# Performance work log

Measured on AMD Instinct MI355X. Metric: run time of the kernel, lower is better.

The kernel has to match this reference:

```python
import jax, jax.numpy as jnp
import numpy as np

B, T, C_M, C_Z, H = 4, 1024, 256, 128, 8
DH = C_M // H  # dim_head = 32


def setup_inputs() -> dict:
    key = jax.random.key(0)
    ks = jax.random.split(key, 6)
    x = jax.random.normal(ks[0], (B, T, C_M), dtype=jnp.float32)
    bias_rep = jax.random.normal(ks[1], (T, T, C_Z), dtype=jnp.float32)
    s = 0.02
    Wqkv = jax.random.normal(ks[2], (C_M, 4 * H * DH), dtype=jnp.float32) * s
    W0 = jax.random.normal(ks[3], (H * DH, C_M), dtype=jnp.float32) * s
    Wb = jax.random.normal(ks[4], (C_Z, H), dtype=jnp.float32) * s
    bb = jax.random.normal(ks[5], (H,), dtype=jnp.float32) * s
    return {"x": x, "bias_rep": bias_rep, "Wqkv": Wqkv, "W0": W0, "Wb": Wb, "bb": bb}


def reference(x, bias_rep, Wqkv, W0, Wb, bb):
    b, t, _ = x.shape
    qkv = x @ Wqkv  # [b, t, 4*H*DH]
    # torch rearrange 'b t (d k h) -> k b h t d' with k=4, h=H: inner layout (d, k, h)
    qkv = qkv.reshape(b, t, DH, 4, H).transpose(3, 0, 4, 1, 2)  # [4, b, H, t, DH]
    q, k, v, g = qkv[0], qkv[1], qkv[2], qkv[3]
    scale = DH ** -0.5
    scores = jnp.einsum('bhid,bhjd->bhij', q, k) * scale  # [b, H, t, t]
    pair_bias = (bias_rep @ Wb + bb)  # [t, t, H]
    pair_bias = pair_bias.transpose(2, 0, 1)[None]  # [1, H, t, t]
    attn = jax.nn.softmax(scores + pair_bias, axis=-1)
    out = jnp.einsum('bhij,bhjd->bhid', attn, v)  # [b, H, t, DH]
    out = out * jax.nn.sigmoid(g)
    out = out.transpose(0, 2, 1, 3).reshape(b, t, H * DH)  # 'b h t d -> b t (h d)'
    return out @ W0
```

## Files before the change

### kernel.cpp

```cpp
#include <hip/hip_runtime.h>
#include <math.h>

#define T_SEQ 1024
#define CM 256
#define HEADS 8
#define DHH 32
#define NB 4

typedef __attribute__((ext_vector_type(8))) short bf16x8;
typedef __attribute__((ext_vector_type(4))) float f32x4;

__device__ __forceinline__ unsigned short f2bf(float f) {
    unsigned u = __builtin_bit_cast(unsigned, f);
    unsigned r = (u + 0x7FFFu + ((u >> 16) & 1u)) >> 16;
    return (unsigned short)r;
}

__global__ __launch_bounds__(256) void cast_x_kernel(const float* __restrict__ x,
                                                     unsigned short* __restrict__ xb) {
    int i = blockIdx.x * 256 + threadIdx.x;
    float4 v = *(const float4*)&x[i * 4];
    ushort4 o;
    o.x = f2bf(v.x); o.y = f2bf(v.y); o.z = f2bf(v.z); o.w = f2bf(v.w);
    *(ushort4*)&xb[i * 4] = o;
}

__global__ __launch_bounds__(256) void transpose_cast_kernel(const float* __restrict__ W,
                                                             unsigned short* __restrict__ Wt,
                                                             int cols) {
    int o = blockIdx.x * 256 + threadIdx.x;
    int n = o >> 8, k = o & 255;
    Wt[o] = f2bf(W[k * cols + n]);
}

__global__ __launch_bounds__(256) void qkv_gemm_mfma(const unsigned short* __restrict__ xb,
                                                     const unsigned short* __restrict__ Wt,
                                                     unsigned short* __restrict__ qb,
                                                     unsigned short* __restrict__ kb,
                                                     unsigned short* __restrict__ vT,
                                                     float* __restrict__ g) {
    const int tid = threadIdx.x;
    const int w = tid >> 6;
    const int lane = tid & 63;
    const int n16 = lane & 15;
    const int quad = lane >> 4;
    const int m0 = blockIdx.y * 64 + w * 16;
    const int hbase = blockIdx.x * 2;
    const float scale = 0.17677669529663687f;

    bf16x8 afr[8];
    #pragma unroll
    for (int kc = 0; kc < 8; ++kc)
        afr[kc] = *(const bf16x8*)&xb[(m0 + n16) * 256 + kc * 32 + quad * 8];

    #pragma unroll
    for (int s = 0; s < 16; ++s) {
        const int h = hbase + (s >> 3);
        const int kk = (s >> 1) & 3;
        const int dhi = s & 1;
        const int c = (dhi * 16 + n16) * 32 + kk * 8 + h;
        f32x4 acc = {0.f, 0.f, 0.f, 0.f};
        #pragma unroll
        for (int kc = 0; kc < 8; ++kc) {
            bf16x8 bfr = *(const bf16x8*)&Wt[c * 256 + kc * 32 + quad * 8];
            acc = __builtin_amdgcn_mfma_f32_16x16x32_bf16(afr[kc], bfr, acc, 0, 0, 0);
        }
        const int d = dhi * 16 + n16;
        #pragma unroll
        for (int r = 0; r < 4; ++r) {
            int m = m0 + quad * 4 + r;
            int b = m >> 10, t = m & 1023;
            int bh = b * HEADS + h;
            float val = acc[r];
            if (kk == 0)      qb[(bh * T_SEQ + t) * DHH + d] = f2bf(val * scale);
            else if (kk == 1) kb[(bh * T_SEQ + t) * DHH + d] = f2bf(val);
            else if (kk == 2) vT[(bh * DHH + d) * T_SEQ + t] = f2bf(val);
            else              g[(bh * T_SEQ + t) * DHH + d] = val;
        }
    }
}

__global__ __launch_bounds__(256) void pair_bias_kernel(const float* __restrict__ bias_rep,
                                                        const float* __restrict__ Wb,
                                                        const float* __restrict__ bb,
                                                        float* __restrict__ pb) {
    __shared__ float wLds[8 * 128];
    __shared__ float outLds[8][64];
    const int tid = threadIdx.x;
    for (int idx = tid; idx < 1024; idx += 256) {
        int c = idx & 127, h = idx >> 7;
        wLds[h * 128 + c] = Wb[c * 8 + h];
    }
    __syncthreads();
    const int group = tid >> 5;
    const int lane32 = tid & 31;
    const int cbase = lane32 * 4;
    const long long p0 = (long long)blockIdx.x * 64;
    for (int it = 0; it < 8; ++it) {
        long long p = p0 + it * 8 + group;
        float4 bv = *(const float4*)&bias_rep[p * 128 + cbase];
        float acc[8];
        #pragma unroll
        for (int h = 0; h < 8; ++h) {
            float4 ww = *(const float4*)&wLds[h * 128 + cbase];
            acc[h] = bv.x * ww.x + bv.y * ww.y + bv.z * ww.z + bv.w * ww.w;
        }
        #pragma unroll
        for (int off = 16; off >= 1; off >>= 1)
            #pragma unroll
            for (int h = 0; h < 8; ++h)
                acc[h] += __shfl_xor(acc[h], off);
        if (lane32 == 0)
            #pragma unroll
            for (int h = 0; h < 8; ++h)
                outLds[h][it * 8 + group] = acc[h] + bb[h];
    }
    __syncthreads();
    for (int idx = tid; idx < 512; idx += 256) {
        int h = idx >> 6, pp = idx & 63;
        pb[(long long)h * (T_SEQ * T_SEQ) + p0 + pp] = outLds[h][pp];
    }
}

__global__ __launch_bounds__(256) void attn_mfma(const unsigned short* __restrict__ qb,
                                                 const unsigned short* __restrict__ kb,
                                                 const unsigned short* __restrict__ vT,
                                                 const float* __restrict__ g,
                                                 const float* __restrict__ pb,
                                                 unsigned short* __restrict__ gated) {
    __shared__ unsigned short Ps[4][16][72];
    const int tid = threadIdx.x;
    const int w = tid >> 6;
    const int lane = tid & 63;
    const int n16 = lane & 15;
    const int quad = lane >> 4;
    const int it0 = blockIdx.x * 64;
    const int h = blockIdx.y, b = blockIdx.z;
    const int bh = b * HEADS + h;
    const int qrow0 = it0 + w * 16;

    bf16x8 qfr = *(const bf16x8*)&qb[(bh * T_SEQ + qrow0 + n16) * DHH + quad * 8];

    float m_i[4] = {-INFINITY, -INFINITY, -INFINITY, -INFINITY};
    float l_i[4] = {0.f, 0.f, 0.f, 0.f};
    f32x4 O0 = {0.f, 0.f, 0.f, 0.f};
    f32x4 O1 = {0.f, 0.f, 0.f, 0.f};

    for (int jt = 0; jt < 16; ++jt) {
        const int j0 = jt * 64;
        f32x4 S[4];
        #pragma unroll
        for (int s4 = 0; s4 < 4; ++s4) {
            bf16x8 kfr = *(const bf16x8*)&kb[(bh * T_SEQ + j0 + s4 * 16 + n16) * DHH + quad * 8];
            f32x4 z = {0.f, 0.f, 0.f, 0.f};
            S[s4] = __builtin_amdgcn_mfma_f32_16x16x32_bf16(qfr, kfr, z, 0, 0, 0);
        }
        #pragma unroll
        for (int s4 = 0; s4 < 4; ++s4)
            #pragma unroll
            for (int r = 0; r < 4; ++r)
                S[s4][r] += pb[h * (T_SEQ * T_SEQ) + (qrow0 + quad * 4 + r) * T_SEQ + j0 + s4 * 16 + n16];
        #pragma unroll
        for (int r = 0; r < 4; ++r) {
            float mx = fmaxf(fmaxf(S[0][r], S[1][r]), fmaxf(S[2][r], S[3][r]));
            mx = fmaxf(mx, __shfl_xor(mx, 1));
            mx = fmaxf(mx, __shfl_xor(mx, 2));
            mx = fmaxf(mx, __shfl_xor(mx, 4));
            mx = fmaxf(mx, __shfl_xor(mx, 8));
            float mnew = fmaxf(m_i[r], mx);
            float alpha = __expf(m_i[r] - mnew);
            m_i[r] = mnew;
            float sum = 0.f;
            #pragma unroll
            for (int s4 = 0; s4 < 4; ++s4) {
                float p = __expf(S[s4][r] - mnew);
                S[s4][r] = p;
                sum += p;
            }
            sum += __shfl_xor(sum, 1);
            sum += __shfl_xor(sum, 2);
            sum += __shfl_xor(sum, 4);
            sum += __shfl_xor(sum, 8);
            l_i[r] = l_i[r] * alpha + sum;
            O0[r] *= alpha;
            O1[r] *= alpha;
        }
        #pragma unroll
        for (int s4 = 0; s4 < 4; ++s4)
            #pragma unroll
            for (int r = 0; r < 4; ++r)
                Ps[w][quad * 4 + r][s4 * 16 + n16] = f2bf(S[s4][r]);
        #pragma unroll
        for (int kc = 0; kc < 2; ++kc) {
            bf16x8 pfr = *(const bf16x8*)&Ps[w][n16][kc * 32 + quad * 8];
            bf16x8 v0 = *(const bf16x8*)&vT[(bh * DHH + n16) * T_SEQ + j0 + kc * 32 + quad * 8];
            bf16x8 v1 = *(const bf16x8*)&vT[(bh * DHH + 16 + n16) * T_SEQ + j0 + kc * 32 + quad * 8];
            O0 = __builtin_amdgcn_mfma_f32_16x16x32_bf16(pfr, v0, O0, 0, 0, 0);
            O1 = __builtin_amdgcn_mfma_f32_16x16x32_bf16(pfr, v1, O1, 0, 0, 0);
        }
    }
    #pragma unroll
    for (int r = 0; r < 4; ++r) {
        int t = qrow0 + quad * 4 + r;
        float linv = 1.f / l_i[r];
        float g0 = g[(bh * T_SEQ + t) * DHH + n16];
        float g1 = g[(bh * T_SEQ + t) * DHH + 16 + n16];
        float o0 = O0[r] * linv / (1.f + __expf(-g0));
        float o1 = O1[r] * linv / (1.f + __expf(-g1));
        gated[(b * T_SEQ + t) * CM + h * DHH + n16] = f2bf(o0);
        gated[(b * T_SEQ + t) * CM + h * DHH + 16 + n16] = f2bf(o1);
    }
}

__global__ __launch_bounds__(64) void out_gemm_mfma(const unsigned short* __restrict__ gb,
                                                    const unsigned short* __restrict__ W0t,
                                                    float* __restrict__ y) {
    const int lane = threadIdx.x;
    const int n16 = lane & 15;
    const int quad = lane >> 4;
    const int m0 = blockIdx.x * 16;

    bf16x8 afr[8];
    #pragma unroll
    for (int kc = 0; kc < 8; ++kc)
        afr[kc] = *(const bf16x8*)&gb[(m0 + n16) * 256 + kc * 32 + quad * 8];

    #pragma unroll
    for (int s = 0; s < 16; ++s) {
        f32x4 acc = {0.f, 0.f, 0.f, 0.f};
        #pragma unroll
        for (int kc = 0; kc < 8; ++kc) {
            bf16x8 bfr = *(const bf16x8*)&W0t[(s * 16 + n16) * 256 + kc * 32 + quad * 8];
            acc = __builtin_amdgcn_mfma_f32_16x16x32_bf16(afr[kc], bfr, acc, 0, 0, 0);
        }
        #pragma unroll
        for (int r = 0; r < 4; ++r)
            y[(m0 + quad * 4 + r) * 256 + s * 16 + n16] = acc[r];
    }
}

extern "C" void kernel_launch(void* const* d_in, const int* in_sizes, int n_in,
                              void* d_out, int out_size, void* d_ws, size_t ws_size,
                              hipStream_t stream) {
    const float* x        = (const float*)d_in[0];
    const float* bias_rep = (const float*)d_in[1];
    const float* Wqkv     = (const float*)d_in[2];
    const float* W0       = (const float*)d_in[3];
    const float* Wb       = (const float*)d_in[4];
    const float* bb       = (const float*)d_in[5];

    char* ws = (char*)d_ws;
    float*          pb    = (float*)ws;                 ws += 8LL * 1024 * 1024 * 4;
    float*          g     = (float*)ws;                 ws += 4LL * 1024 * 1024;
    unsigned short* qb    = (unsigned short*)ws;        ws += 2LL * 1024 * 1024;
    unsigned short* kb    = (unsigned short*)ws;        ws += 2LL * 1024 * 1024;
    unsigned short* vT    = (unsigned short*)ws;        ws += 2LL * 1024 * 1024;
    unsigned short* gated = (unsigned short*)ws;        ws += 2LL * 1024 * 1024;
    unsigned short* xb    = (unsigned short*)ws;        ws += 2LL * 1024 * 1024;
    unsigned short* Wt    = (unsigned short*)ws;        ws += 512LL * 1024;
    unsigned short* W0t   = (unsigned short*)ws;
    float* y = (float*)d_out;

    cast_x_kernel<<<1024, 256, 0, stream>>>(x, xb);
    transpose_cast_kernel<<<1024, 256, 0, stream>>>(Wqkv, Wt, 1024);
    transpose_cast_kernel<<<256, 256, 0, stream>>>(W0, W0t, 256);
    qkv_gemm_mfma<<<dim3(4, 64), 256, 0, stream>>>(xb, Wt, qb, kb, vT, g);
    pair_bias_kernel<<<dim3(16384), 256, 0, stream>>>(bias_rep, Wb, bb, pb);
    attn_mfma<<<dim3(16, HEADS, NB), 256, 0, stream>>>(qb, kb, vT, g, pb, gated);
    out_gemm_mfma<<<256, 64, 0, stream>>>(gated, W0t, y);
}
```

Measured before the change: 884.1 us.

## Use MFMA for pair bias, fuse x cast into QKV GEMM, tune attention loop

The pair-bias projection moves from scalar dot products with shuffle reductions to bf16 MFMA against a zero-padded transposed Wb. The separate x cast kernel is removed: the QKV GEMM now loads fp32 x and converts it in registers, and its grid doubles to one head per block. In attention, pair-bias loads are issued before the QK MFMAs, s_setprio brackets the MFMA sections, and the per-tile row-sum shuffle reduction is deferred to the epilogue. Rounding bias_rep to bf16 lowers precision in the pair-bias term.

```diff
diff --git a/kernel.cpp b/kernel.cpp
--- a/kernel.cpp
+++ b/kernel.cpp
@@ -6,6 +6,7 @@
 #define HEADS 8
 #define DHH 32
 #define NB 4
+#define TT (T_SEQ * T_SEQ)
 
 typedef __attribute__((ext_vector_type(8))) short bf16x8;
 typedef __attribute__((ext_vector_type(4))) float f32x4;
@@ -16,13 +17,13 @@
     return (unsigned short)r;
 }
 
-__global__ __launch_bounds__(256) void cast_x_kernel(const float* __restrict__ x,
-                                                     unsigned short* __restrict__ xb) {
-    int i = blockIdx.x * 256 + threadIdx.x;
-    float4 v = *(const float4*)&x[i * 4];
-    ushort4 o;
-    o.x = f2bf(v.x); o.y = f2bf(v.y); o.z = f2bf(v.z); o.w = f2bf(v.w);
-    *(ushort4*)&xb[i * 4] = o;
+__device__ __forceinline__ bf16x8 cvt8(const float4 a0, const float4 a1) {
+    bf16x8 t;
+    t[0] = (short)f2bf(a0.x); t[1] = (short)f2bf(a0.y);
+    t[2] = (short)f2bf(a0.z); t[3] = (short)f2bf(a0.w);
+    t[4] = (short)f2bf(a1.x); t[5] = (short)f2bf(a1.y);
+    t[6] = (short)f2bf(a1.z); t[7] = (short)f2bf(a1.w);
+    return t;
 }
 
 __global__ __launch_bounds__(256) void transpose_cast_kernel(const float* __restrict__ W,
@@ -33,7 +34,14 @@
     Wt[o] = f2bf(W[k * cols + n]);
 }
 
-__global__ __launch_bounds__(256) void qkv_gemm_mfma(const unsigned short* __restrict__ xb,
+__global__ __launch_bounds__(256) void pad_wb_kernel(const float* __restrict__ Wb,
+                                                     unsigned short* __restrict__ WbT) {
+    int idx = blockIdx.x * 256 + threadIdx.x;
+    int h = idx >> 7, k = idx & 127;
+    WbT[idx] = (h < 8) ? f2bf(Wb[k * 8 + h]) : (unsigned short)0;
+}
+
+__global__ __launch_bounds__(256) void qkv_gemm_mfma(const float* __restrict__ x,
                                                      const unsigned short* __restrict__ Wt,
                                                      unsigned short* __restrict__ qb,
                                                      unsigned short* __restrict__ kb,
@@ -45,18 +53,21 @@
     const int n16 = lane & 15;
     const int quad = lane >> 4;
     const int m0 = blockIdx.y * 64 + w * 16;
-    const int hbase = blockIdx.x * 2;
+    const int h = blockIdx.x;
     const float scale = 0.17677669529663687f;
 
     bf16x8 afr[8];
     #pragma unroll
-    for (int kc = 0; kc < 8; ++kc)
-        afr[kc] = *(const bf16x8*)&xb[(m0 + n16) * 256 + kc * 32 + quad * 8];
-
-    #pragma unroll
-    for (int s = 0; s < 16; ++s) {
-        const int h = hbase + (s >> 3);
-        const int kk = (s >> 1) & 3;
+    for (int kc = 0; kc < 8; ++kc) {
+        const float* src = &x[(m0 + n16) * 256 + kc * 32 + quad * 8];
+        float4 a0 = *(const float4*)src;
+        float4 a1 = *(const float4*)(src + 4);
+        afr[kc] = cvt8(a0, a1);
+    }
+
+    #pragma unroll
+    for (int s = 0; s < 8; ++s) {
+        const int kk = s >> 1;
         const int dhi = s & 1;
         const int c = (dhi * 16 + n16) * 32 + kk * 8 + h;
         f32x4 acc = {0.f, 0.f, 0.f, 0.f};
@@ -80,45 +91,38 @@
     }
 }
 
-__global__ __launch_bounds__(256) void pair_bias_kernel(const float* __restrict__ bias_rep,
-                                                        const float* __restrict__ Wb,
-                                                        const float* __restrict__ bb,
-                                                        float* __restrict__ pb) {
-    __shared__ float wLds[8 * 128];
-    __shared__ float outLds[8][64];
+__global__ __launch_bounds__(256) void pair_bias_mfma(const float* __restrict__ bias_rep,
+                                                      const unsigned short* __restrict__ WbT,
+                                                      const float* __restrict__ bb,
+                                                      float* __restrict__ pb) {
     const int tid = threadIdx.x;
-    for (int idx = tid; idx < 1024; idx += 256) {
-        int c = idx & 127, h = idx >> 7;
-        wLds[h * 128 + c] = Wb[c * 8 + h];
-    }
-    __syncthreads();
-    const int group = tid >> 5;
-    const int lane32 = tid & 31;
-    const int cbase = lane32 * 4;
-    const long long p0 = (long long)blockIdx.x * 64;
-    for (int it = 0; it < 8; ++it) {
-        long long p = p0 + it * 8 + group;
-        float4 bv = *(const float4*)&bias_rep[p * 128 + cbase];
-        float acc[8];
-        #pragma unroll
-        for (int h = 0; h < 8; ++h) {
-            float4 ww = *(const float4*)&wLds[h * 128 + cbase];
-            acc[h] = bv.x * ww.x + bv.y * ww.y + bv.z * ww.z + bv.w * ww.w;
-        }
-        #pragma unroll
-        for (int off = 16; off >= 1; off >>= 1)
-            #pragma unroll
-            for (int h = 0; h < 8; ++h)
-                acc[h] += __shfl_xor(acc[h], off);
-        if (lane32 == 0)
-            #pragma unroll
-            for (int h = 0; h < 8; ++h)
-                outLds[h][it * 8 + group] = acc[h] + bb[h];
-    }
-    __syncthreads();
-    for (int idx = tid; idx < 512; idx += 256) {
-        int h = idx >> 6, pp = idx & 63;
-        pb[(long long)h * (T_SEQ * T_SEQ) + p0 + pp] = outLds[h][pp];
+    const int w = tid >> 6;
+    const int lane = tid & 63;
+    const int n16 = lane & 15;
+    const int quad = lane >> 4;
+    const int p0 = blockIdx.x * 64 + w * 16;
+
+    bf16x8 afr[4];
+    #pragma unroll
+    for (int kc = 0; kc < 4; ++kc) {
+        const float* src = &bias_rep[(long long)(p0 + n16) * 128 + kc * 32 + quad * 8];
+        float4 a0 = *(const float4*)src;
+        float4 a1 = *(const float4*)(src + 4);
+        afr[kc] = cvt8(a0, a1);
+    }
+
+    f32x4 acc = {0.f, 0.f, 0.f, 0.f};
+    #pragma unroll
+    for (int kc = 0; kc < 4; ++kc) {
+        bf16x8 bfr = *(const bf16x8*)&WbT[n16 * 128 + kc * 32 + quad * 8];
+        acc = __builtin_amdgcn_mfma_f32_16x16x32_bf16(afr[kc], bfr, acc, 0, 0, 0);
+    }
+
+    if (n16 < 8) {
+        float bbv = bb[n16];
+        #pragma unroll
+        for (int r = 0; r < 4; ++r)
+            pb[(long long)n16 * TT + p0 + quad * 4 + r] = acc[r] + bbv;
     }
 }
 
@@ -148,18 +152,29 @@
 
     for (int jt = 0; jt < 16; ++jt) {
         const int j0 = jt * 64;
+        float pbv[4][4];
+        #pragma unroll
+        for (int s4 = 0; s4 < 4; ++s4)
+            #pragma unroll
+            for (int r = 0; r < 4; ++r)
+                pbv[s4][r] = pb[h * TT + (qrow0 + quad * 4 + r) * T_SEQ + j0 + s4 * 16 + n16];
+
         f32x4 S[4];
+        __builtin_amdgcn_s_setprio(1);
         #pragma unroll
         for (int s4 = 0; s4 < 4; ++s4) {
             bf16x8 kfr = *(const bf16x8*)&kb[(bh * T_SEQ + j0 + s4 * 16 + n16) * DHH + quad * 8];
             f32x4 z = {0.f, 0.f, 0.f, 0.f};
             S[s4] = __builtin_amdgcn_mfma_f32_16x16x32_bf16(qfr, kfr, z, 0, 0, 0);
         }
+        __builtin_amdgcn_s_setprio(0);
+
         #pragma unroll
         for (int s4 = 0; s4 < 4; ++s4)
             #pragma unroll
             for (int r = 0; r < 4; ++r)
-                S[s4][r] += pb[h * (T_SEQ * T_SEQ) + (qrow0 + quad * 4 + r) * T_SEQ + j0 + s4 * 16 + n16];
+                S[s4][r] += pbv[s4][r];
+
         #pragma unroll
         for (int r = 0; r < 4; ++r) {
             float mx = fmaxf(fmaxf(S[0][r], S[1][r]), fmaxf(S[2][r], S[3][r]));
@@ -170,26 +185,24 @@
             float mnew = fmaxf(m_i[r], mx);
             float alpha = __expf(m_i[r] - mnew);
             m_i[r] = mnew;
-            float sum = 0.f;
+            float lsum = 0.f;
             #pragma unroll
             for (int s4 = 0; s4 < 4; ++s4) {
                 float p = __expf(S[s4][r] - mnew);
                 S[s4][r] = p;
-                sum += p;
+                lsum += p;
             }
-            sum += __shfl_xor(sum, 1);
-            sum += __shfl_xor(sum, 2);
-            sum += __shfl_xor(sum, 4);
-            sum += __shfl_xor(sum, 8);
-            l_i[r] = l_i[r] * alpha + sum;
+            l_i[r] = l_i[r] * alpha + lsum;
             O0[r] *= alpha;
             O1[r] *= alpha;
         }
+
         #pragma unroll
         for (int s4 = 0; s4 < 4; ++s4)
             #pragma unroll
             for (int r = 0; r < 4; ++r)
                 Ps[w][quad * 4 + r][s4 * 16 + n16] = f2bf(S[s4][r]);
+        __builtin_amdgcn_s_setprio(1);
         #pragma unroll
         for (int kc = 0; kc < 2; ++kc) {
             bf16x8 pfr = *(const bf16x8*)&Ps[w][n16][kc * 32 + quad * 8];
@@ -198,11 +211,18 @@
             O0 = __builtin_amdgcn_mfma_f32_16x16x32_bf16(pfr, v0, O0, 0, 0, 0);
             O1 = __builtin_amdgcn_mfma_f32_16x16x32_bf16(pfr, v1, O1, 0, 0, 0);
         }
-    }
+        __builtin_amdgcn_s_setprio(0);
+    }
+
     #pragma unroll
     for (int r = 0; r < 4; ++r) {
+        float lr = l_i[r];
+        lr += __shfl_xor(lr, 1);
+        lr += __shfl_xor(lr, 2);
+        lr += __shfl_xor(lr, 4);
+        lr += __shfl_xor(lr, 8);
         int t = qrow0 + quad * 4 + r;
-        float linv = 1.f / l_i[r];
+        float linv = 1.f / lr;
         float g0 = g[(bh * T_SEQ + t) * DHH + n16];
         float g1 = g[(bh * T_SEQ + t) * DHH + 16 + n16];
         float o0 = O0[r] * linv / (1.f + __expf(-g0));
@@ -256,16 +276,16 @@
     unsigned short* kb    = (unsigned short*)ws;        ws += 2LL * 1024 * 1024;
     unsigned short* vT    = (unsigned short*)ws;        ws += 2LL * 1024 * 1024;
     unsigned short* gated = (unsigned short*)ws;        ws += 2LL * 1024 * 1024;
-    unsigned short* xb    = (unsigned short*)ws;        ws += 2LL * 1024 * 1024;
     unsigned short* Wt    = (unsigned short*)ws;        ws += 512LL * 1024;
-    unsigned short* W0t   = (unsigned short*)ws;
+    unsigned short* W0t   = (unsigned short*)ws;        ws += 128LL * 1024;
+    unsigned short* WbT   = (unsigned short*)ws;
     float* y = (float*)d_out;
 
-    cast_x_kernel<<<1024, 256, 0, stream>>>(x, xb);
     transpose_cast_kernel<<<1024, 256, 0, stream>>>(Wqkv, Wt, 1024);
     transpose_cast_kernel<<<256, 256, 0, stream>>>(W0, W0t, 256);
-    qkv_gemm_mfma<<<dim3(4, 64), 256, 0, stream>>>(xb, Wt, qb, kb, vT, g);
-    pair_bias_kernel<<<dim3(16384), 256, 0, stream>>>(bias_rep, Wb, bb, pb);
+    pad_wb_kernel<<<8, 256, 0, stream>>>(Wb, WbT);
+    qkv_gemm_mfma<<<dim3(8, 64), 256, 0, stream>>>(x, Wt, qb, kb, vT, g);
+    pair_bias_mfma<<<16384, 256, 0, stream>>>(bias_rep, WbT, bb, pb);
     attn_mfma<<<dim3(16, HEADS, NB), 256, 0, stream>>>(qb, kb, vT, g, pb, gated);
     out_gemm_mfma<<<256, 64, 0, stream>>>(gated, W0t, y);
 }
```

New measurement: 804.3 us. 1.1x faster.
